# Kernel optimization log

Measured on AMD Instinct MI355X. Metric: run time of the kernel, lower is better.

The kernel has to match this reference:

```python
import jax, jax.numpy as jnp
import numpy as np

D_MODEL = 256
HEADS = 4
HEAD_DIM = D_MODEL // HEADS  # 64
BN_EPS = 1e-5


def conv1(x, W, b):
    # Conv1d kernel_size=1 == per-position linear: x [B,C,N], W [O,C], b [O]
    return jnp.einsum('oc,bcn->bon', W, x) + b[:, None]


def setup_inputs() -> dict:
    key = jax.random.key(0)
    ks = jax.random.split(key, 12)
    B, N, M = 4, 4096, 4096
    s = 0.02
    return {
        'x': jax.random.normal(ks[0], (B, D_MODEL, N), jnp.float32),
        'source': jax.random.normal(ks[1], (B, D_MODEL, M), jnp.float32),
        'pq_w': jax.random.normal(ks[2], (D_MODEL, D_MODEL), jnp.float32) * s,
        'pq_b': jnp.zeros((D_MODEL,), jnp.float32),
        'pk_w': jax.random.normal(ks[3], (D_MODEL, D_MODEL), jnp.float32) * s,
        'pk_b': jnp.zeros((D_MODEL,), jnp.float32),
        'pv_w': jax.random.normal(ks[4], (D_MODEL, D_MODEL), jnp.float32) * s,
        'pv_b': jnp.zeros((D_MODEL,), jnp.float32),
        'merge_w': jax.random.normal(ks[5], (D_MODEL, D_MODEL), jnp.float32) * s,
        'merge_b': jnp.zeros((D_MODEL,), jnp.float32),
        'mlp1_w': jax.random.normal(ks[6], (2 * D_MODEL, 2 * D_MODEL), jnp.float32) * s,
        'mlp1_b': jax.random.normal(ks[7], (2 * D_MODEL,), jnp.float32) * s,
        'bn_gamma': jnp.ones((2 * D_MODEL,), jnp.float32),
        'bn_beta': jnp.zeros((2 * D_MODEL,), jnp.float32),
        'mlp2_w': jax.random.normal(ks[8], (D_MODEL, 2 * D_MODEL), jnp.float32) * s,
        'mlp2_b': jnp.zeros((D_MODEL,), jnp.float32),  # nn.init.constant_(mlp[-1].bias, 0.0)
    }


def reference(x, source, pq_w, pq_b, pk_w, pk_b, pv_w, pv_b,
              merge_w, merge_b, mlp1_w, mlp1_b, bn_gamma, bn_beta,
              mlp2_w, mlp2_b):
    B = x.shape[0]
    # projections; torch view(B, dim, heads, -1): channels split as (head_dim, heads)
    q = conv1(x, pq_w, pq_b).reshape(B, HEAD_DIM, HEADS, -1)       # [B,d,h,N]
    k = conv1(source, pk_w, pk_b).reshape(B, HEAD_DIM, HEADS, -1)  # [B,d,h,M]
    v = conv1(source, pv_w, pv_b).reshape(B, HEAD_DIM, HEADS, -1)
    scores = jnp.einsum('bdhn,bdhm->bhnm', q, k) / (HEAD_DIM ** 0.5)
    prob = jax.nn.softmax(scores, axis=-1)                          # [B,h,N,M]
    attn_out = jnp.einsum('bhnm,bdhm->bdhn', prob, v).reshape(B, D_MODEL, -1)
    message = conv1(attn_out, merge_w, merge_b)                     # [B,D,N]
    # MLP: conv(512->512) + BatchNorm1d (training-mode batch stats) + ReLU + conv(512->256)
    h = conv1(jnp.concatenate([x, message], axis=1), mlp1_w, mlp1_b)  # [B,2D,N]
    mean = jnp.mean(h, axis=(0, 2), keepdims=True)
    var = jnp.var(h, axis=(0, 2), keepdims=True)  # biased, as torch BN uses for normalization
    h = bn_gamma[:, None] * (h - mean) * jax.lax.rsqrt(var + BN_EPS) + bn_beta[:, None]
    h = jax.nn.relu(h)
    return conv1(h, mlp2_w, mlp2_b)
```

## Files before the change

kernel.cpp:

```cpp
#include <hip/hip_runtime.h>
#include <hip/hip_bf16.h>

#define D_MODEL 256
#define HEADS 4
#define HD 64
#define BATCH 4
#define SEQ 4096
#define NPOS (BATCH*SEQ)
#define SCALE_LOG2 0.18033688011112042f
#define MCHUNKS 2

typedef __attribute__((ext_vector_type(4))) float floatx4;
typedef __attribute__((ext_vector_type(8))) short bf16x8;
typedef __attribute__((ext_vector_type(4))) short bf16x4;
typedef __attribute__((ext_vector_type(4))) unsigned short ushortx4;

__device__ __forceinline__ float bf2f(unsigned short b) {
    return __uint_as_float(((unsigned int)b) << 16);
}
__device__ __forceinline__ unsigned short f2bf(float f) {
    unsigned int u = __float_as_uint(f);
    return (unsigned short)((u + 0x7fffu + ((u >> 16) & 1u)) >> 16);
}
__device__ __forceinline__ bf16x4 pack_bf16x4(float a, float b, float c, float d) {
    __hip_bfloat162 lo = __float22bfloat162_rn(float2{a, b});
    __hip_bfloat162 hi = __float22bfloat162_rn(float2{c, d});
    union { __hip_bfloat162 h2[2]; bf16x4 v; } u;
    u.h2[0] = lo; u.h2[1] = hi;
    return u.v;
}
__device__ __forceinline__ bf16x8 pack_bf16x8(floatx4 a, floatx4 b) {
    union { bf16x4 h[2]; bf16x8 v; } u;
    u.h[0] = pack_bf16x4(a[0], a[1], a[2], a[3]);
    u.h[1] = pack_bf16x4(b[0], b[1], b[2], b[3]);
    return u.v;
}
#define MFMA(a,b,c) __builtin_amdgcn_mfma_f32_16x16x32_bf16((a),(b),(c),0,0,0)
#define EXP2(x) __builtin_amdgcn_exp2f(x)

__global__ __launch_bounds__(256) void prep(
        const float* __restrict__ pq_w, const float* __restrict__ pk_w,
        const float* __restrict__ pv_w, const float* __restrict__ merge_w,
        const float* __restrict__ mlp1_w, const float* __restrict__ mlp2_w,
        const float* __restrict__ x, const float* __restrict__ src,
        unsigned short* __restrict__ wqb, unsigned short* __restrict__ wkb,
        unsigned short* __restrict__ wvb, unsigned short* __restrict__ wmt,
        unsigned short* __restrict__ w1b, unsigned short* __restrict__ w2b,
        unsigned short* __restrict__ xT, unsigned short* __restrict__ srcT)
{
    __shared__ unsigned short lT[64][264];
    const int t = threadIdx.x;
    const int bx = blockIdx.x;
    if (bx < 576) {
        int linear = bx * 1024 + t * 4;
        const float* srcW; unsigned short* dst; int off;
        if (linear < 65536)       { srcW = pq_w;   dst = wqb; off = 0; }
        else if (linear < 131072) { srcW = pk_w;   dst = wkb; off = 65536; }
        else if (linear < 196608) { srcW = pv_w;   dst = wvb; off = 131072; }
        else if (linear < 458752) { srcW = mlp1_w; dst = w1b; off = 196608; }
        else                      { srcW = mlp2_w; dst = w2b; off = 458752; }
        int i = linear - off;
        float4 w = *(const float4*)&srcW[i];
        ushortx4 s = { f2bf(w.x), f2bf(w.y), f2bf(w.z), f2bf(w.w) };
        *(ushortx4*)&dst[i] = s;
        return;
    }
    if (bx < 640) {
        int i = (bx - 576) * 1024 + t * 4;
        int cp = i >> 8, o = i & 255;
        int pc = ((cp & 63) << 2) | (cp >> 6);
        unsigned short s[4];
#pragma unroll
        for (int j = 0; j < 4; ++j)
            s[j] = f2bf(merge_w[(size_t)(o + j) * 256 + pc]);
        *(ushortx4*)&wmt[i] = *(const ushortx4*)s;
        return;
    }
    int z = bx - 640;
    const float* X = (z < 256) ? x : src;
    unsigned short* O = (z < 256) ? xT : srcT;
    int rem = z & 255;
    int b = rem >> 6, n0 = (rem & 63) * 64;
#pragma unroll
    for (int r = 0; r < 16; ++r) {
        int idx = r * 256 + t;
        int ch = idx >> 4, nnq = (idx & 15) * 4;
        float4 v4 = *(const float4*)&X[((size_t)b * 256 + ch) * SEQ + n0 + nnq];
        lT[nnq + 0][ch] = f2bf(v4.x);
        lT[nnq + 1][ch] = f2bf(v4.y);
        lT[nnq + 2][ch] = f2bf(v4.z);
        lT[nnq + 3][ch] = f2bf(v4.w);
    }
    __syncthreads();
#pragma unroll
    for (int r = 0; r < 8; ++r) {
        int idx = r * 256 + t;
        int row = idx >> 5, cg = (idx & 31) * 8;
        *(bf16x8*)&O[((size_t)b * SEQ + n0 + row) * 256 + cg] = *(const bf16x8*)&lT[row][cg];
    }
}

__global__ __launch_bounds__(256) void prep2(
        const float* __restrict__ mlp1_w, const float* __restrict__ mlp1_b,
        const float* __restrict__ merge_b, const unsigned short* __restrict__ wmt,
        unsigned short* __restrict__ w1f, float* __restrict__ b1f)
{
    __shared__ unsigned short lA[64][40];
    __shared__ unsigned short lB[128][40];
    const int t = threadIdx.x;
    if (blockIdx.y == 8) {
        int o2 = blockIdx.x * 256 + t;
        float s = mlp1_b[o2];
        for (int o = 0; o < 256; ++o)
            s += mlp1_w[(size_t)o2 * 512 + 256 + o] * merge_b[o];
        b1f[o2] = s;
        return;
    }
    const int lane = t & 63, wid = t >> 6;
    const int wm = wid >> 1, wn = wid & 1;
    const int lrow = lane & 15, quad = lane >> 4;
    const int o20 = blockIdx.y * 64;
    const int c0  = blockIdx.x * 128;

    floatx4 acc[2][4];
#pragma unroll
    for (int i = 0; i < 2; ++i)
#pragma unroll
        for (int j = 0; j < 4; ++j) acc[i][j] = (floatx4){0.f,0.f,0.f,0.f};

    for (int k0 = 0; k0 < 256; k0 += 32) {
#pragma unroll
        for (int r = 0; r < 2; ++r) {
            int linear = r * 1024 + t * 4;
            int row = linear >> 5, col = linear & 31;
            float4 w = *(const float4*)&mlp1_w[(size_t)(o20 + row) * 512 + 256 + k0 + col];
            ushortx4 s = { f2bf(w.x), f2bf(w.y), f2bf(w.z), f2bf(w.w) };
            *(ushortx4*)&lA[row][col] = s;
        }
#pragma unroll
        for (int r = 0; r < 2; ++r) {
            int linear = r * 256 + t;
            int row = linear >> 2, cg = (linear & 3) * 8;
            *(bf16x8*)&lB[row][cg] = *(const bf16x8*)&wmt[(size_t)(c0 + row) * 256 + k0 + cg];
        }
        __syncthreads();
        bf16x8 aF[2], bF[4];
        const int kq = quad * 8;
#pragma unroll
        for (int mt = 0; mt < 2; ++mt)
            aF[mt] = *(const bf16x8*)&lA[wm*32 + mt*16 + lrow][kq];
#pragma unroll
        for (int nt = 0; nt < 4; ++nt)
            bF[nt] = *(const bf16x8*)&lB[wn*64 + nt*16 + lrow][kq];
#pragma unroll
        for (int mt = 0; mt < 2; ++mt)
#pragma unroll
            for (int nt = 0; nt < 4; ++nt)
                acc[mt][nt] = MFMA(aF[mt], bF[nt], acc[mt][nt]);
        __syncthreads();
    }
#pragma unroll
    for (int nt = 0; nt < 4; ++nt) {
        int cp = c0 + wn*64 + nt*16 + lrow;
#pragma unroll
        for (int mt = 0; mt < 2; ++mt)
#pragma unroll
            for (int j = 0; j < 4; ++j) {
                int o2 = o20 + wm*32 + mt*16 + quad*4 + j;
                w1f[(size_t)o2 * 256 + cp] = f2bf(acc[mt][nt][j]);
            }
    }
}

__global__ __launch_bounds__(256) void proj_qkv_all(
        const unsigned short* __restrict__ Wq, const float* __restrict__ bq,
        const unsigned short* __restrict__ Wk, const float* __restrict__ bk,
        const unsigned short* __restrict__ Wv, const float* __restrict__ bv,
        const unsigned short* __restrict__ xT, const unsigned short* __restrict__ srcT,
        unsigned short* __restrict__ qo, unsigned short* __restrict__ ko,
        unsigned short* __restrict__ vo)
{
    __shared__ unsigned short smem[128 * 80];
    unsigned short (*lA)[40] = (unsigned short (*)[40])smem;
    unsigned short (*lB)[40] = (unsigned short (*)[40])(smem + 128 * 40);
    unsigned short (*stage)[72] = (unsigned short (*)[72])smem;
    unsigned short* stage2 = smem;
    const int t = threadIdx.x;
    const int lane = t & 63, wid = t >> 6;
    const int wm = wid >> 1, wn = wid & 1;
    const int lrow = lane & 15, quad = lane >> 4;
    const int mode = blockIdx.x >> 1;
    const int ob = (blockIdx.x & 1) * 128;
    const int n0 = blockIdx.y * 128;
    const int b  = blockIdx.z;
    const unsigned short* W  = (mode == 0) ? Wq : (mode == 1) ? Wk : Wv;
    const float* bias        = (mode == 0) ? bq : (mode == 1) ? bk : bv;
    const unsigned short* XT = (mode == 0) ? xT : srcT;
    unsigned short* out      = (mode == 0) ? qo : (mode == 1) ? ko : vo;

    const int srow[2] = { (0*256 + t) >> 2, (1*256 + t) >> 2 };
    const int scg = (t & 3) * 8;

    floatx4 acc[4][4];
#pragma unroll
    for (int i = 0; i < 4; ++i)
#pragma unroll
        for (int j = 0; j < 4; ++j) acc[i][j] = (floatx4){0.f,0.f,0.f,0.f};

    bf16x8 rW[2], rX[2];
#pragma unroll
    for (int r = 0; r < 2; ++r) {
        rW[r] = *(const bf16x8*)&W[(size_t)(ob + srow[r]) * 256 + scg];
        rX[r] = *(const bf16x8*)&XT[((size_t)b * SEQ + n0 + srow[r]) * 256 + scg];
    }
#pragma unroll
    for (int r = 0; r < 2; ++r) {
        *(bf16x8*)&lA[srow[r]][scg] = rW[r];
        *(bf16x8*)&lB[srow[r]][scg] = rX[r];
    }
    __syncthreads();

    for (int kc = 0; kc < 8; ++kc) {
        const bool pre = (kc + 1 < 8);
        if (pre) {
            const int k1 = (kc + 1) * 32;
#pragma unroll
            for (int r = 0; r < 2; ++r) {
                rW[r] = *(const bf16x8*)&W[(size_t)(ob + srow[r]) * 256 + k1 + scg];
                rX[r] = *(const bf16x8*)&XT[((size_t)b * SEQ + n0 + srow[r]) * 256 + k1 + scg];
            }
        }
        bf16x8 aF[4], bF[4];
        const int kq = quad * 8;
#pragma unroll
        for (int mt = 0; mt < 4; ++mt)
            aF[mt] = *(const bf16x8*)&lA[wm*64 + mt*16 + lrow][kq];
#pragma unroll
        for (int nt = 0; nt < 4; ++nt)
            bF[nt] = *(const bf16x8*)&lB[wn*64 + nt*16 + lrow][kq];
#pragma unroll
        for (int mt = 0; mt < 4; ++mt)
#pragma unroll
            for (int nt = 0; nt < 4; ++nt)
                acc[mt][nt] = MFMA(aF[mt], bF[nt], acc[mt][nt]);
        __syncthreads();
        if (pre) {
#pragma unroll
            for (int r = 0; r < 2; ++r) {
                *(bf16x8*)&lA[srow[r]][scg] = rW[r];
                *(bf16x8*)&lB[srow[r]][scg] = rX[r];
            }
            __syncthreads();
        }
    }
    const float osc = (mode == 0) ? SCALE_LOG2 : 1.0f;
    if (mode == 2) {
        for (int half = 0; half < 2; ++half) {
            __syncthreads();
            if (wm == half) {
#pragma unroll
                for (int mt = 0; mt < 4; ++mt)
#pragma unroll
                    for (int j = 0; j < 4; ++j) {
                        int ol = mt*16 + quad*4 + j;
                        float bvv = bias[ob + half*64 + ol];
#pragma unroll
                        for (int nt = 0; nt < 4; ++nt) {
                            int n = wn*64 + nt*16 + lrow;
                            stage2[ol*132 + n] = f2bf(acc[mt][nt][j] + bvv);
                        }
                    }
            }
            __syncthreads();
#pragma unroll
            for (int i = 0; i < 4; ++i) {
                int c = i * 256 + t;
                int row = c >> 4, sub = c & 15;
                int o = ob + half*64 + row;
                int d = o >> 2, h = o & 3;
                *(bf16x8*)&out[((size_t)(b*HEADS + h) * HD + d) * SEQ + n0 + sub*8] =
                    *(const bf16x8*)&stage2[row*132 + sub*8];
            }
        }
        return;
    }
    for (int half = 0; half < 2; ++half) {
        __syncthreads();
        if (wm == half) {
#pragma unroll
            for (int mt = 0; mt < 4; ++mt)
#pragma unroll
                for (int j = 0; j < 4; ++j) {
                    int o = ob + half*64 + mt*16 + quad*4 + j;
                    float bvv = bias[o];
                    int col = j*16 + mt*4 + quad;
#pragma unroll
                    for (int nt = 0; nt < 4; ++nt) {
                        int n = wn*64 + nt*16 + lrow;
                        stage[n][col] = f2bf((acc[mt][nt][j] + bvv) * osc);
                    }
                }
        }
        __syncthreads();
#pragma unroll
        for (int i = 0; i < 4; ++i) {
            int c = i * 256 + t;
            int n = c >> 3, h = (c >> 1) & 3, sub = c & 1;
            bf16x8 val = *(const bf16x8*)&stage[n][h*16 + sub*8];
            int d0 = (ob >> 2) + half*16 + sub*8;
            *(bf16x8*)&out[((size_t)(b*HEADS + h) * SEQ + n0 + n) * HD + d0] = val;
        }
    }
}

__global__ __launch_bounds__(256, 4) void flash_attn(
        const unsigned short* __restrict__ q,
        const unsigned short* __restrict__ k,
        const unsigned short* __restrict__ v,
        unsigned short* __restrict__ poO, float* __restrict__ pol)
{
    __shared__ unsigned short smem[2][8192];
    const int t = threadIdx.x, lane = t & 63, wid = t >> 6;
    const int lrow = lane & 15, quad = lane >> 4;
    const int xq = lane & 7;
    const int bc = blockIdx.x, qt = blockIdx.y;
    const int bh = bc & 15, chunk = bc >> 4;
    const int hb = (bh & 3) * BATCH + (bh >> 2);
    const int r0 = qt * 128 + wid * 32;

    bf16x8 qf[2][2];
#pragma unroll
    for (int nh = 0; nh < 2; ++nh) {
        const size_t base = ((size_t)bh * SEQ + r0 + nh*16 + lrow) * HD;
        qf[nh][0] = *(const bf16x8*)&q[base + quad * 8];
        qf[nh][1] = *(const bf16x8*)&q[base + 32 + quad * 8];
    }
    bf16x8 ones;
#pragma unroll
    for (int i = 0; i < 8; ++i) ones[i] = (short)0x3F80;
    int mmv[2], cgv[2], kwo[2], vwo[2];
#pragma unroll
    for (int r = 0; r < 2; ++r) {
        int linear = r * 256 + t;
        int mm = linear >> 3, cg = (linear & 7) * 8;
        int c2 = mm >> 5, mp = mm & 31;
        int krv = (c2 << 5) + ((mp & 4) << 2) + ((mp >> 3) << 2) + (mp & 3);
        mmv[r] = mm; cgv[r] = cg;
        kwo[r] = krv * 64 + (((cg >> 3) ^ (krv & 7)) << 3);
        vwo[r] = 4096 + mm * 64 + (((cg >> 3) ^ (mm & 7)) << 3);
    }
    const size_t kbase = ((size_t)bh * SEQ + chunk * (SEQ/MCHUNKS));
    const size_t vbase = (size_t)bh * HD;
    const int moff = chunk * (SEQ/MCHUNKS);
    const int NIT = SEQ / MCHUNKS / 64;

    floatx4 oacc[2][4], oaccL[2];
#pragma unroll
    for (int nh = 0; nh < 2; ++nh) {
        oaccL[nh] = (floatx4){0.f,0.f,0.f,0.f};
#pragma unroll
        for (int i = 0; i < 4; ++i) oacc[nh][i] = (floatx4){0.f,0.f,0.f,0.f};
    }

    {
        bf16x8 pk[2], pv[2];
#pragma unroll
        for (int r = 0; r < 2; ++r) {
            pk[r] = *(const bf16x8*)&k[(kbase + mmv[r]) * HD + cgv[r]];
            pv[r] = *(const bf16x8*)&v[(vbase + mmv[r]) * SEQ + moff + cgv[r]];
        }
#pragma unroll
        for (int r = 0; r < 2; ++r) {
            *(bf16x8*)&smem[0][kwo[r]] = pk[r];
            *(bf16x8*)&smem[0][vwo[r]] = pv[r];
        }
    }
    __syncthreads();

    int p = 0;
#pragma unroll 1
    for (int it = 0; it < NIT; ++it) {
        bf16x8 pk[2], pv[2];
        const bool pre = (it + 1 < NIT);
        if (pre) {
            const int m1 = (it + 1) * 64;
#pragma unroll
            for (int r = 0; r < 2; ++r) {
                pk[r] = *(const bf16x8*)&k[(kbase + m1 + mmv[r]) * HD + cgv[r]];
                pv[r] = *(const bf16x8*)&v[(vbase + mmv[r]) * SEQ + moff + m1 + cgv[r]];
            }
        }
        const unsigned short* lS = smem[p];

        bf16x8 pf8[2][2];
#pragma unroll
        for (int c2 = 0; c2 < 2; ++c2) {
            floatx4 sa[2][2];
#pragma unroll
            for (int AB = 0; AB < 2; ++AB) {
                sa[AB][0] = (floatx4){0.f,0.f,0.f,0.f};
                sa[AB][1] = (floatx4){0.f,0.f,0.f,0.f};
            }
            __builtin_amdgcn_s_setprio(1);
#pragma unroll
            for (int AB = 0; AB < 2; ++AB) {
#pragma unroll
                for (int kc = 0; kc < 2; ++kc) {
                    bf16x8 kf = *(const bf16x8*)&lS[(c2*32 + AB*16 + lrow)*64
                                                    + (((kc*4 + quad) ^ xq) << 3)];
                    sa[AB][0] = MFMA(kf, qf[0][kc], sa[AB][0]);
                    sa[AB][1] = MFMA(kf, qf[1][kc], sa[AB][1]);
                }
            }
            __builtin_amdgcn_s_setprio(0);
#pragma unroll
            for (int nh = 0; nh < 2; ++nh) {
                floatx4 ea, eb;
#pragma unroll
                for (int i = 0; i < 4; ++i) { ea[i] = EXP2(sa[0][nh][i]); eb[i] = EXP2(sa[1][nh][i]); }
                pf8[c2][nh] = pack_bf16x8(ea, eb);
            }
        }
        __builtin_amdgcn_s_setprio(1);
#pragma unroll
        for (int c2 = 0; c2 < 2; ++c2) {
            oaccL[0] = MFMA(ones, pf8[c2][0], oaccL[0]);
            oaccL[1] = MFMA(ones, pf8[c2][1], oaccL[1]);
#pragma unroll
            for (int dt = 0; dt < 4; ++dt) {
                bf16x8 vf = *(const bf16x8*)&lS[4096 + (dt*16 + lrow)*64
                                                + (((c2*4 + quad) ^ xq) << 3)];
                oacc[0][dt] = MFMA(vf, pf8[c2][0], oacc[0][dt]);
                oacc[1][dt] = MFMA(vf, pf8[c2][1], oacc[1][dt]);
            }
        }
        __builtin_amdgcn_s_setprio(0);
        if (pre) {
#pragma unroll
            for (int r = 0; r < 2; ++r) {
                *(bf16x8*)&smem[p^1][kwo[r]] = pk[r];
                *(bf16x8*)&smem[p^1][vwo[r]] = pv[r];
            }
        }
        __syncthreads();
        p ^= 1;
    }
    const size_t prow = (size_t)(chunk*16 + hb) * SEQ + qt * 128;
    if (lane < 16) {
        pol[prow + wid*32 + lrow]      = oaccL[0][0];
        pol[prow + wid*32 + 16 + lrow] = oaccL[1][0];
    }
    unsigned short* stB = (unsigned short*)&smem[0][0];
#pragma unroll
    for (int nh = 0; nh < 2; ++nh)
#pragma unroll
        for (int dt = 0; dt < 4; ++dt) {
            bf16x4 pv4 = pack_bf16x4(oacc[nh][dt][0], oacc[nh][dt][1],
                                     oacc[nh][dt][2], oacc[nh][dt][3]);
            int row = wid*32 + nh*16 + lrow;
            int blk = dt*2 + (quad >> 1);
            *(bf16x4*)&stB[row*64 + ((blk ^ xq) << 3) + (quad & 1)*4] = pv4;
        }
    __syncthreads();
#pragma unroll
    for (int i = 0; i < 4; ++i) {
        int c = i * 256 + t;
        int row = c >> 3, sub = c & 7;
        *(bf16x8*)&poO[(prow + row) * HD + sub*8] =
            *(const bf16x8*)&stB[row*64 + ((sub ^ (row & 7)) << 3)];
    }
}

__global__ __launch_bounds__(256) void gemm_mlp1(
        const unsigned short* __restrict__ xT, const unsigned short* __restrict__ poO,
        const float* __restrict__ pol,
        const unsigned short* __restrict__ w1b, const unsigned short* __restrict__ w1f,
        const float* __restrict__ b1f, unsigned short* __restrict__ h1,
        float* __restrict__ sums, float* __restrict__ sumsq)
{
    __shared__ unsigned short lA[2][64][40];
    __shared__ unsigned short lB[2][128][40];
    __shared__ float sInv[256];
    const int t = threadIdx.x;
    const int lane = t & 63, wid = t >> 6;
    const int wm = wid >> 1, wn = wid & 1;
    const int lrow = lane & 15, quad = lane >> 4;
    const int o0 = blockIdx.x * 128;
    const int p0 = blockIdx.y * 64;
    const int b = p0 >> 12, n0 = p0 & (SEQ - 1);
    const size_t CH = (size_t)16 * SEQ * HD;

    {
        int h = t >> 6, nn = t & 63;
        int hb = h * BATCH + b;
        float l = 0.f;
#pragma unroll
        for (int c = 0; c < MCHUNKS; ++c)
            l += pol[((size_t)(c*16 + hb)) * SEQ + n0 + nn];
        sInv[t] = 1.0f / l;
    }
    __syncthreads();

    const int arow = t >> 2, acg = (t & 3) * 8;
    const int brow[2] = { (0*256 + t) >> 2, (1*256 + t) >> 2 };

    floatx4 acc[2][4];
#pragma unroll
    for (int i = 0; i < 2; ++i)
#pragma unroll
        for (int j = 0; j < 4; ++j) acc[i][j] = (floatx4){0.f,0.f,0.f,0.f};

    bf16x8 rA, rB[2];
    auto load_tile = [&](int k0) {
        if (k0 < 256) {
            rA = *(const bf16x8*)&xT[(size_t)(p0 + arow) * 256 + k0 + acg];
#pragma unroll
            for (int r = 0; r < 2; ++r)
                rB[r] = *(const bf16x8*)&w1b[(size_t)(o0 + brow[r]) * 512 + k0 + acg];
        } else {
            const int kk2 = k0 - 256;
            const int h = kk2 >> 6, d0 = kk2 & 63, hb = h * BATCH + b;
            const unsigned short* bse = &poO[((size_t)hb * SEQ + n0 + arow) * HD + d0 + acg];
            float inv = sInv[h*64 + arow];
            float fs[8];
#pragma unroll
            for (int i = 0; i < 8; ++i) fs[i] = 0.f;
#pragma unroll
            for (int c = 0; c < MCHUNKS; ++c) {
                bf16x8 a = *(const bf16x8*)(bse + (size_t)c * CH);
#pragma unroll
                for (int i = 0; i < 8; ++i)
                    fs[i] += bf2f((unsigned short)a[i]);
            }
            unsigned short res[8];
#pragma unroll
            for (int i = 0; i < 8; ++i)
                res[i] = f2bf(fs[i] * inv);
            rA = *(const bf16x8*)res;
#pragma unroll
            for (int r = 0; r < 2; ++r)
                rB[r] = *(const bf16x8*)&w1f[(size_t)(o0 + brow[r]) * 256 + kk2 + acg];
        }
    };

    load_tile(0);
    *(bf16x8*)&lA[0][arow][acg] = rA;
#pragma unroll
    for (int r = 0; r < 2; ++r) *(bf16x8*)&lB[0][brow[r]][acg] = rB[r];
    __syncthreads();

    int p = 0;
    for (int kc = 0; kc < 16; ++kc) {
        const bool pre = (kc + 1 < 16);
        if (pre) load_tile((kc + 1) * 32);
        bf16x8 aF[2], bF[4];
        const int kq = quad * 8;
#pragma unroll
        for (int mt = 0; mt < 2; ++mt)
            aF[mt] = *(const bf16x8*)&lA[p][wm*32 + mt*16 + lrow][kq];
#pragma unroll
        for (int nt = 0; nt < 4; ++nt)
            bF[nt] = *(const bf16x8*)&lB[p][wn*64 + nt*16 + lrow][kq];
#pragma unroll
        for (int mt = 0; mt < 2; ++mt)
#pragma unroll
            for (int nt = 0; nt < 4; ++nt)
                acc[mt][nt] = MFMA(aF[mt], bF[nt], acc[mt][nt]);
        if (pre) {
            *(bf16x8*)&lA[p^1][arow][acg] = rA;
#pragma unroll
            for (int r = 0; r < 2; ++r) *(bf16x8*)&lB[p^1][brow[r]][acg] = rB[r];
        }
        __syncthreads();
        p ^= 1;
    }
#pragma unroll
    for (int nt = 0; nt < 4; ++nt) {
        int o = o0 + wn*64 + nt*16 + lrow;
        float bvv = b1f[o];
        float s = 0.f, qs = 0.f;
#pragma unroll
        for (int mt = 0; mt < 2; ++mt)
#pragma unroll
            for (int j = 0; j < 4; ++j) {
                int pos = p0 + wm*32 + mt*16 + quad*4 + j;
                float val = acc[mt][nt][j] + bvv;
                h1[(size_t)pos * 512 + o] = f2bf(val);
                s += val; qs += val * val;
            }
        s  += __shfl_xor(s, 16);  s  += __shfl_xor(s, 32);
        qs += __shfl_xor(qs, 16); qs += __shfl_xor(qs, 32);
        if (lane < 16) {
            atomicAdd(&sums[o], s);
            atomicAdd(&sumsq[o], qs);
        }
    }
}

__global__ __launch_bounds__(256) void gemm_mlp2(
        const unsigned short* __restrict__ W2, const unsigned short* __restrict__ h1,
        const float* __restrict__ bias,
        const float* __restrict__ sums, const float* __restrict__ sumsq,
        const float* __restrict__ gamma, const float* __restrict__ beta,
        float* __restrict__ out)
{
    __shared__ unsigned short lA[2][128][40];
    __shared__ unsigned short lB[2][64][40];
    __shared__ float sSc[512], sSh[512];
    const int t = threadIdx.x;
    const int lane = t & 63, wid = t >> 6;
    const int wm = wid >> 1, wn = wid & 1;
    const int lrow = lane & 15, quad = lane >> 4;
    const int o0 = blockIdx.x * 128;
    const int p0 = blockIdx.y * 64;

#pragma unroll
    for (int cc = 0; cc < 2; ++cc) {
        int c = cc * 256 + t;
        float mean = sums[c] * (1.0f / NPOS);
        float var  = sumsq[c] * (1.0f / NPOS) - mean * mean;
        float sc = gamma[c] * rsqrtf(var + 1e-5f);
        sSc[c] = sc;
        sSh[c] = beta[c] - mean * sc;
    }
    __syncthreads();

    const int arow[2] = { (0*256 + t) >> 2, (1*256 + t) >> 2 };
    const int acg = (t & 3) * 8;
    const int brow = t >> 2;

    floatx4 acc[4][2];
#pragma unroll
    for (int i = 0; i < 4; ++i)
#pragma unroll
        for (int j = 0; j < 2; ++j) acc[i][j] = (floatx4){0.f,0.f,0.f,0.f};

    bf16x8 rW[2], rH;
    auto load_tile = [&](int k0) {
#pragma unroll
        for (int r = 0; r < 2; ++r)
            rW[r] = *(const bf16x8*)&W2[(size_t)(o0 + arow[r]) * 512 + k0 + acg];
        bf16x8 hv = *(const bf16x8*)&h1[(size_t)(p0 + brow) * 512 + k0 + acg];
        unsigned short res[8];
#pragma unroll
        for (int i = 0; i < 8; ++i) {
            int c = k0 + acg + i;
            float f = bf2f((unsigned short)hv[i]);
            f = fmaxf(f * sSc[c] + sSh[c], 0.f);
            res[i] = f2bf(f);
        }
        rH = *(const bf16x8*)res;
    };

    load_tile(0);
#pragma unroll
    for (int r = 0; r < 2; ++r) *(bf16x8*)&lA[0][arow[r]][acg] = rW[r];
    *(bf16x8*)&lB[0][brow][acg] = rH;
    __syncthreads();

    int p = 0;
    for (int kc = 0; kc < 16; ++kc) {
        const bool pre = (kc + 1 < 16);
        if (pre) load_tile((kc + 1) * 32);
        bf16x8 aF[4], bF[2];
        const int kq = quad * 8;
#pragma unroll
        for (int mt = 0; mt < 4; ++mt)
            aF[mt] = *(const bf16x8*)&lA[p][wm*64 + mt*16 + lrow][kq];
#pragma unroll
        for (int nt = 0; nt < 2; ++nt)
            bF[nt] = *(const bf16x8*)&lB[p][wn*32 + nt*16 + lrow][kq];
#pragma unroll
        for (int mt = 0; mt < 4; ++mt)
#pragma unroll
            for (int nt = 0; nt < 2; ++nt)
                acc[mt][nt] = MFMA(aF[mt], bF[nt], acc[mt][nt]);
        if (pre) {
#pragma unroll
            for (int r = 0; r < 2; ++r) *(bf16x8*)&lA[p^1][arow[r]][acg] = rW[r];
            *(bf16x8*)&lB[p^1][brow][acg] = rH;
        }
        __syncthreads();
        p ^= 1;
    }
#pragma unroll
    for (int mt = 0; mt < 4; ++mt)
#pragma unroll
        for (int j = 0; j < 4; ++j) {
            int o = o0 + wm*64 + mt*16 + quad*4 + j;
            float bvv = bias[o];
#pragma unroll
            for (int nt = 0; nt < 2; ++nt) {
                int pos = p0 + wn*32 + nt*16 + lrow;
                int b = pos >> 12, n = pos & (SEQ - 1);
                out[((size_t)b * D_MODEL + o) * SEQ + n] = acc[mt][nt][j] + bvv;
            }
        }
}

extern "C" void kernel_launch(void* const* d_in, const int* in_sizes, int n_in,
                              void* d_out, int out_size, void* d_ws, size_t ws_size,
                              hipStream_t stream)
{
    (void)in_sizes; (void)n_in; (void)out_size; (void)ws_size;
    const float* x        = (const float*)d_in[0];
    const float* source   = (const float*)d_in[1];
    const float* pq_w     = (const float*)d_in[2];
    const float* pq_b     = (const float*)d_in[3];
    const float* pk_w     = (const float*)d_in[4];
    const float* pk_b     = (const float*)d_in[5];
    const float* pv_w     = (const float*)d_in[6];
    const float* pv_b     = (const float*)d_in[7];
    const float* merge_w  = (const float*)d_in[8];
    const float* merge_b  = (const float*)d_in[9];
    const float* mlp1_w   = (const float*)d_in[10];
    const float* mlp1_b   = (const float*)d_in[11];
    const float* bn_gamma = (const float*)d_in[12];
    const float* bn_beta  = (const float*)d_in[13];
    const float* mlp2_w   = (const float*)d_in[14];
    const float* mlp2_b   = (const float*)d_in[15];
    float* out = (float*)d_out;

    char* ws = (char*)d_ws;
    const size_t MB = 1ull << 20;
    unsigned short* xT   = (unsigned short*)(ws);
    unsigned short* srcT = (unsigned short*)(ws + 8*MB);
    unsigned short* q    = (unsigned short*)(ws + 16*MB);
    unsigned short* kk   = (unsigned short*)(ws + 24*MB);
    unsigned short* v    = (unsigned short*)(ws + 32*MB);
    unsigned short* poO  = (unsigned short*)(ws + 40*MB);
    unsigned short* h1   = (unsigned short*)(ws + 16*MB);
    float* pol = (float*)(ws + 72*MB);
    unsigned short* wqb = (unsigned short*)(ws + 73*MB);
    unsigned short* wkb = wqb + 65536;
    unsigned short* wvb = wkb + 65536;
    unsigned short* wmt = wvb + 65536;
    unsigned short* w1b = wmt + 65536;
    unsigned short* w2b = w1b + 262144;
    unsigned short* w1f = w2b + 131072;
    float* b1f = (float*)(w1f + 131072);
    float* bn_sum = b1f + 512;
    float* bn_sumsq = bn_sum + 512;

    hipMemsetAsync(bn_sum, 0, 1024 * sizeof(float), stream);

    prep<<<dim3(1152), 256, 0, stream>>>(
        pq_w, pk_w, pv_w, merge_w, mlp1_w, mlp2_w, x, source,
        wqb, wkb, wvb, wmt, w1b, w2b, xT, srcT);
    prep2<<<dim3(2, 9), 256, 0, stream>>>(mlp1_w, mlp1_b, merge_b, wmt, w1f, b1f);
    proj_qkv_all<<<dim3(6, SEQ/128, BATCH), 256, 0, stream>>>(
        wqb, pq_b, wkb, pk_b, wvb, pv_b, xT, srcT, q, kk, v);
    flash_attn<<<dim3(16*MCHUNKS, SEQ/128), 256, 0, stream>>>(q, kk, v, poO, pol);
    gemm_mlp1<<<dim3(4, NPOS/64), 256, 0, stream>>>(
        xT, poO, pol, w1b, w1f, b1f, h1, bn_sum, bn_sumsq);
    gemm_mlp2<<<dim3(2, NPOS/64), 256, 0, stream>>>(
        w2b, h1, mlp2_b, bn_sum, bn_sumsq, bn_gamma, bn_beta, out);
}
```

Before: 278.5 us.

## Double query rows per flash-attention wave and switch LDS to padded layout

Each wave in the flash attention kernel now handles 64 query rows instead of 32, and each block handles 256 rows, so every K/V tile loaded into shared memory feeds twice as many MFMAs. The grid shrinks to half as many blocks. The LDS layout changes from XOR-swizzled rows of 64 to padded rows of 72 elements, and the stage buffer grows to match. The cost is more accumulator registers, hence launch bounds of 2 blocks per CU, and fewer blocks to hide latency and balance work across CUs.

New measurement: 253.8 us. -8.9%, faster.

```diff
diff --git a/kernel.cpp b/kernel.cpp
--- a/kernel.cpp
+++ b/kernel.cpp
@@ -313,24 +313,23 @@
     }
 }
 
-__global__ __launch_bounds__(256, 4) void flash_attn(
+__global__ __launch_bounds__(256, 2) void flash_attn(
         const unsigned short* __restrict__ q,
         const unsigned short* __restrict__ k,
         const unsigned short* __restrict__ v,
         unsigned short* __restrict__ poO, float* __restrict__ pol)
 {
-    __shared__ unsigned short smem[2][8192];
+    __shared__ unsigned short smem[2][9216];
     const int t = threadIdx.x, lane = t & 63, wid = t >> 6;
     const int lrow = lane & 15, quad = lane >> 4;
-    const int xq = lane & 7;
     const int bc = blockIdx.x, qt = blockIdx.y;
     const int bh = bc & 15, chunk = bc >> 4;
     const int hb = (bh & 3) * BATCH + (bh >> 2);
-    const int r0 = qt * 128 + wid * 32;
-
-    bf16x8 qf[2][2];
-#pragma unroll
-    for (int nh = 0; nh < 2; ++nh) {
+    const int r0 = qt * 256 + wid * 64;
+
+    bf16x8 qf[4][2];
+#pragma unroll
+    for (int nh = 0; nh < 4; ++nh) {
         const size_t base = ((size_t)bh * SEQ + r0 + nh*16 + lrow) * HD;
         qf[nh][0] = *(const bf16x8*)&q[base + quad * 8];
         qf[nh][1] = *(const bf16x8*)&q[base + 32 + quad * 8];
@@ -338,25 +337,23 @@
     bf16x8 ones;
 #pragma unroll
     for (int i = 0; i < 8; ++i) ones[i] = (short)0x3F80;
-    int mmv[2], cgv[2], kwo[2], vwo[2];
+    int mmv[2], cgv[2], krv[2];
 #pragma unroll
     for (int r = 0; r < 2; ++r) {
         int linear = r * 256 + t;
         int mm = linear >> 3, cg = (linear & 7) * 8;
         int c2 = mm >> 5, mp = mm & 31;
-        int krv = (c2 << 5) + ((mp & 4) << 2) + ((mp >> 3) << 2) + (mp & 3);
         mmv[r] = mm; cgv[r] = cg;
-        kwo[r] = krv * 64 + (((cg >> 3) ^ (krv & 7)) << 3);
-        vwo[r] = 4096 + mm * 64 + (((cg >> 3) ^ (mm & 7)) << 3);
+        krv[r] = (c2 << 5) + ((mp & 4) << 2) + ((mp >> 3) << 2) + (mp & 3);
     }
     const size_t kbase = ((size_t)bh * SEQ + chunk * (SEQ/MCHUNKS));
     const size_t vbase = (size_t)bh * HD;
     const int moff = chunk * (SEQ/MCHUNKS);
     const int NIT = SEQ / MCHUNKS / 64;
 
-    floatx4 oacc[2][4], oaccL[2];
-#pragma unroll
-    for (int nh = 0; nh < 2; ++nh) {
+    floatx4 oacc[4][4], oaccL[4];
+#pragma unroll
+    for (int nh = 0; nh < 4; ++nh) {
         oaccL[nh] = (floatx4){0.f,0.f,0.f,0.f};
 #pragma unroll
         for (int i = 0; i < 4; ++i) oacc[nh][i] = (floatx4){0.f,0.f,0.f,0.f};
@@ -371,8 +368,8 @@
         }
 #pragma unroll
         for (int r = 0; r < 2; ++r) {
-            *(bf16x8*)&smem[0][kwo[r]] = pk[r];
-            *(bf16x8*)&smem[0][vwo[r]] = pv[r];
+            *(bf16x8*)&smem[0][krv[r]*72 + cgv[r]]        = pk[r];
+            *(bf16x8*)&smem[0][4608 + mmv[r]*72 + cgv[r]] = pv[r];
         }
     }
     __syncthreads();
@@ -392,82 +389,78 @@
         }
         const unsigned short* lS = smem[p];
 
-        bf16x8 pf8[2][2];
 #pragma unroll
         for (int c2 = 0; c2 < 2; ++c2) {
-            floatx4 sa[2][2];
+            floatx4 sa[2][4];
+#pragma unroll
+            for (int AB = 0; AB < 2; ++AB)
+#pragma unroll
+                for (int nh = 0; nh < 4; ++nh)
+                    sa[AB][nh] = (floatx4){0.f,0.f,0.f,0.f};
+            __builtin_amdgcn_s_setprio(1);
 #pragma unroll
             for (int AB = 0; AB < 2; ++AB) {
-                sa[AB][0] = (floatx4){0.f,0.f,0.f,0.f};
-                sa[AB][1] = (floatx4){0.f,0.f,0.f,0.f};
+#pragma unroll
+                for (int kc = 0; kc < 2; ++kc) {
+                    bf16x8 kf = *(const bf16x8*)&lS[(c2*32 + AB*16 + lrow)*72 + kc*32 + quad*8];
+#pragma unroll
+                    for (int nh = 0; nh < 4; ++nh)
+                        sa[AB][nh] = MFMA(kf, qf[nh][kc], sa[AB][nh]);
+                }
+            }
+            __builtin_amdgcn_s_setprio(0);
+            bf16x8 pf8[4];
+#pragma unroll
+            for (int nh = 0; nh < 4; ++nh) {
+                floatx4 ea, eb;
+#pragma unroll
+                for (int i = 0; i < 4; ++i) { ea[i] = EXP2(sa[0][nh][i]); eb[i] = EXP2(sa[1][nh][i]); }
+                pf8[nh] = pack_bf16x8(ea, eb);
             }
             __builtin_amdgcn_s_setprio(1);
 #pragma unroll
-            for (int AB = 0; AB < 2; ++AB) {
-#pragma unroll
-                for (int kc = 0; kc < 2; ++kc) {
-                    bf16x8 kf = *(const bf16x8*)&lS[(c2*32 + AB*16 + lrow)*64
-                                                    + (((kc*4 + quad) ^ xq) << 3)];
-                    sa[AB][0] = MFMA(kf, qf[0][kc], sa[AB][0]);
-                    sa[AB][1] = MFMA(kf, qf[1][kc], sa[AB][1]);
-                }
+            for (int nh = 0; nh < 4; ++nh)
+                oaccL[nh] = MFMA(ones, pf8[nh], oaccL[nh]);
+#pragma unroll
+            for (int dt = 0; dt < 4; ++dt) {
+                bf16x8 vf = *(const bf16x8*)&lS[4608 + (dt*16 + lrow)*72 + c2*32 + quad*8];
+#pragma unroll
+                for (int nh = 0; nh < 4; ++nh)
+                    oacc[nh][dt] = MFMA(vf, pf8[nh], oacc[nh][dt]);
             }
             __builtin_amdgcn_s_setprio(0);
-#pragma unroll
-            for (int nh = 0; nh < 2; ++nh) {
-                floatx4 ea, eb;
-#pragma unroll
-                for (int i = 0; i < 4; ++i) { ea[i] = EXP2(sa[0][nh][i]); eb[i] = EXP2(sa[1][nh][i]); }
-                pf8[c2][nh] = pack_bf16x8(ea, eb);
-            }
-        }
-        __builtin_amdgcn_s_setprio(1);
-#pragma unroll
-        for (int c2 = 0; c2 < 2; ++c2) {
-            oaccL[0] = MFMA(ones, pf8[c2][0], oaccL[0]);
-            oaccL[1] = MFMA(ones, pf8[c2][1], oaccL[1]);
-#pragma unroll
-            for (int dt = 0; dt < 4; ++dt) {
-                bf16x8 vf = *(const bf16x8*)&lS[4096 + (dt*16 + lrow)*64
-                                                + (((c2*4 + quad) ^ xq) << 3)];
-                oacc[0][dt] = MFMA(vf, pf8[c2][0], oacc[0][dt]);
-                oacc[1][dt] = MFMA(vf, pf8[c2][1], oacc[1][dt]);
-            }
-        }
-        __builtin_amdgcn_s_setprio(0);
+        }
         if (pre) {
 #pragma unroll
             for (int r = 0; r < 2; ++r) {
-                *(bf16x8*)&smem[p^1][kwo[r]] = pk[r];
-                *(bf16x8*)&smem[p^1][vwo[r]] = pv[r];
+                *(bf16x8*)&smem[p^1][krv[r]*72 + cgv[r]]        = pk[r];
+                *(bf16x8*)&smem[p^1][4608 + mmv[r]*72 + cgv[r]] = pv[r];
             }
         }
         __syncthreads();
         p ^= 1;
     }
-    const size_t prow = (size_t)(chunk*16 + hb) * SEQ + qt * 128;
+    const size_t prow = (size_t)(chunk*16 + hb) * SEQ + qt * 256;
     if (lane < 16) {
-        pol[prow + wid*32 + lrow]      = oaccL[0][0];
-        pol[prow + wid*32 + 16 + lrow] = oaccL[1][0];
+#pragma unroll
+        for (int nh = 0; nh < 4; ++nh)
+            pol[prow + wid*64 + nh*16 + lrow] = oaccL[nh][0];
     }
     unsigned short* stB = (unsigned short*)&smem[0][0];
 #pragma unroll
-    for (int nh = 0; nh < 2; ++nh)
+    for (int nh = 0; nh < 4; ++nh)
 #pragma unroll
         for (int dt = 0; dt < 4; ++dt) {
             bf16x4 pv4 = pack_bf16x4(oacc[nh][dt][0], oacc[nh][dt][1],
                                      oacc[nh][dt][2], oacc[nh][dt][3]);
-            int row = wid*32 + nh*16 + lrow;
-            int blk = dt*2 + (quad >> 1);
-            *(bf16x4*)&stB[row*64 + ((blk ^ xq) << 3) + (quad & 1)*4] = pv4;
+            *(bf16x4*)&stB[(wid*64 + nh*16 + lrow)*72 + dt*16 + quad*4] = pv4;
         }
     __syncthreads();
 #pragma unroll
-    for (int i = 0; i < 4; ++i) {
+    for (int i = 0; i < 8; ++i) {
         int c = i * 256 + t;
         int row = c >> 3, sub = c & 7;
-        *(bf16x8*)&poO[(prow + row) * HD + sub*8] =
-            *(const bf16x8*)&stB[row*64 + ((sub ^ (row & 7)) << 3)];
+        *(bf16x8*)&poO[(prow + row) * HD + sub*8] = *(const bf16x8*)&stB[row*72 + sub*8];
     }
 }
 
@@ -750,7 +743,7 @@
     prep2<<<dim3(2, 9), 256, 0, stream>>>(mlp1_w, mlp1_b, merge_b, wmt, w1f, b1f);
     proj_qkv_all<<<dim3(6, SEQ/128, BATCH), 256, 0, stream>>>(
         wqb, pq_b, wkb, pk_b, wvb, pv_b, xT, srcT, q, kk, v);
-    flash_attn<<<dim3(16*MCHUNKS, SEQ/128), 256, 0, stream>>>(q, kk, v, poO, pol);
+    flash_attn<<<dim3(16*MCHUNKS, SEQ/256), 256, 0, stream>>>(q, kk, v, poO, pol);
     gemm_mlp1<<<dim3(4, NPOS/64), 256, 0, stream>>>(
         xT, poO, pol, w1b, w1f, b1f, h1, bn_sum, bn_sumsq);
     gemm_mlp2<<<dim3(2, NPOS/64), 256, 0, stream>>>(
```
